# Kernel tuning notes

Measured on AMD Instinct MI355X. Metric: run time of the kernel, lower is better.

The kernel has to match this reference:

```python
import jax, jax.numpy as jnp
import numpy as np

MARGIN = 1.0
N, D = 8192, 128
NUM_CLASSES = 43


def setup_inputs() -> dict:
    key = jax.random.key(0)
    kx, ky = jax.random.split(key)
    x = jax.random.normal(kx, (N, D), dtype=jnp.float32)
    y = jax.random.randint(ky, (N,), 0, NUM_CLASSES, dtype=jnp.int64)
    return {"x": x, "y": y}


def reference(x, y):
    # Pairwise squared distances between rows of x: [N, N].
    # Equivalent to the original tile/permute construction, but via GEMM:
    # ||a-b||^2 = ||a||^2 + ||b||^2 - 2 a.b
    sq = jnp.sum(x * x, axis=1)                      # [N]
    norms = sq[:, None] + sq[None, :] - 2.0 * (x @ x.T)  # [N, N]
    maxims = jnp.maximum(MARGIN - norms, 0.0)        # [N, N]

    # Same-label mask (1 where labels equal, 0 otherwise).
    equalities = (y[:, None] == y[None, :]).astype(norms.dtype)  # [N, N]
    eye = jnp.eye(x.shape[0], dtype=norms.dtype)

    pos_mask = equalities - eye       # positive pairs, excluding self
    neg_mask = 1.0 - equalities       # negative pairs

    pos_term = jnp.sum(pos_mask * norms) / jnp.sum(pos_mask)
    neg_term = jnp.sum(neg_mask * maxims) / jnp.sum(neg_mask)
    return (pos_term + neg_term) / 2.0
```

## Files before the change

kernel.cpp:

```cpp
#include <hip/hip_runtime.h>

#define N_ROWS 8192
#define DIM 128
#define NCLS 43
#define TILE 256
#define TILES2 32
#define NPAIRS2 528

typedef __attribute__((ext_vector_type(8))) __bf16 bf16x8;
typedef __attribute__((ext_vector_type(4))) float float4v;
typedef __attribute__((address_space(1))) const void global_cvoid;
typedef __attribute__((address_space(3))) void lds_void;

__device__ __forceinline__ unsigned short f2bf(float f) {
    unsigned int u = __float_as_uint(f);
    u += 0x7FFFu + ((u >> 16) & 1u);
    return (unsigned short)(u >> 16);
}

__global__ void __launch_bounds__(256) prep_kernel(
        const float* __restrict__ x,
        float* __restrict__ sq,
        unsigned short* __restrict__ xbf) {
    int wave = threadIdx.x >> 6;
    int lane = threadIdx.x & 63;
    int row  = blockIdx.x * 4 + wave;
    const float2 v = *(const float2*)(x + (size_t)row * DIM + lane * 2);
    ushort2 b; b.x = f2bf(v.x); b.y = f2bf(v.y);
    *(ushort2*)(xbf + (size_t)row * DIM + lane * 2) = b;
    float s = v.x * v.x + v.y * v.y;
    #pragma unroll
    for (int off = 32; off > 0; off >>= 1) s += __shfl_down(s, off);
    if (lane == 0) sq[row] = s;
}

#define SM_B   65536
#define SM_SQA 131072
#define SM_SQB 132096
#define SM_YA  133120
#define SM_YB  134144
#define SM_RED 135168

__global__ void __launch_bounds__(1024, 4) tile_kernel(
        const unsigned short* __restrict__ xbf,
        const float* __restrict__ sq,
        const int* __restrict__ y,
        float2* __restrict__ partials) {
    __shared__ __align__(16) char smem[135296];

    int t = blockIdx.x;
    int bi = (int)((65.0f - sqrtf((float)(65 * 65 - 8 * t))) * 0.5f);
    if (bi < 0) bi = 0;
    if (bi > TILES2 - 1) bi = TILES2 - 1;
    while (bi * TILES2 - (bi * (bi - 1)) / 2 > t) --bi;
    while ((bi + 1) * TILES2 - ((bi + 1) * bi) / 2 <= t) ++bi;
    int bj = bi + (t - (bi * TILES2 - (bi * (bi - 1)) / 2));

    int wv   = threadIdx.x >> 6;
    int lane = threadIdx.x & 63;

    const char* srcA = (const char*)(xbf + (size_t)bi * TILE * DIM);
    const char* srcB = (const char*)(xbf + (size_t)bj * TILE * DIM);
    #pragma unroll
    for (int it = 0; it < 4; ++it) {
        int pbase = (it * 16 + wv) * 1024;
        int p = pbase + lane * 16;
        int r = p >> 8;
        int c = ((p >> 4) & 15) ^ (r & 15);
        int goff = (r << 8) + (c << 4);
        __builtin_amdgcn_global_load_lds(
            (global_cvoid*)(srcA + goff), (lds_void*)(smem + pbase), 16, 0, 0);
        __builtin_amdgcn_global_load_lds(
            (global_cvoid*)(srcB + goff), (lds_void*)(smem + SM_B + pbase), 16, 0, 0);
    }
    {
        int ti = threadIdx.x;
        if (ti < 256)       ((float*)(smem + SM_SQA))[ti]       = sq[bi * TILE + ti];
        else if (ti < 512)  ((float*)(smem + SM_SQB))[ti - 256] = sq[bj * TILE + ti - 256];
        else if (ti < 768)  ((int*)  (smem + SM_YA ))[ti - 512] = y [bi * TILE + ti - 512];
        else                ((int*)  (smem + SM_YB ))[ti - 768] = y [bj * TILE + ti - 768];
    }
    __syncthreads();

    int m    = lane & 15;
    int quad = lane >> 4;
    int wr   = (wv >> 2) * 64;
    int wc   = (wv & 3) * 64;

    float4v acc[4][4];
    #pragma unroll
    for (int a = 0; a < 4; ++a)
        #pragma unroll
        for (int b = 0; b < 4; ++b) {
            float4v z = {0.f, 0.f, 0.f, 0.f};
            acc[a][b] = z;
        }

    #pragma unroll
    for (int ks = 0; ks < 4; ++ks) {
        int chunk = ((ks * 4 + quad) ^ m) * 16;
        bf16x8 af[4], bfr[4];
        #pragma unroll
        for (int ti = 0; ti < 4; ++ti)
            af[ti] = *(const bf16x8*)(smem + (wr + ti * 16 + m) * 256 + chunk);
        #pragma unroll
        for (int tj = 0; tj < 4; ++tj)
            bfr[tj] = *(const bf16x8*)(smem + SM_B + (wc + tj * 16 + m) * 256 + chunk);
        #pragma unroll
        for (int ti = 0; ti < 4; ++ti)
            #pragma unroll
            for (int tj = 0; tj < 4; ++tj)
                acc[ti][tj] = __builtin_amdgcn_mfma_f32_16x16x32_bf16(
                                  af[ti], bfr[tj], acc[ti][tj], 0, 0, 0);
    }

    const float* sqA = (const float*)(smem + SM_SQA);
    const float* sqB = (const float*)(smem + SM_SQB);
    const int*   yA  = (const int*)  (smem + SM_YA);
    const int*   yB  = (const int*)  (smem + SM_YB);
    int ibase = wr + quad * 4;
    int jbase = wc + m;

    float sqj[4]; int yj[4];
    #pragma unroll
    for (int tj = 0; tj < 4; ++tj) {
        sqj[tj] = sqB[jbase + tj * 16];
        yj[tj]  = yB [jbase + tj * 16];
    }
    float posP = 0.f, negP = 0.f;
    if (bi != bj) {
        #pragma unroll
        for (int ti = 0; ti < 4; ++ti) {
            #pragma unroll
            for (int r = 0; r < 4; ++r) {
                int il = ibase + ti * 16 + r;
                float sqi = sqA[il];
                int   yi  = yA [il];
                #pragma unroll
                for (int tj = 0; tj < 4; ++tj) {
                    float nrm = fmaf(-2.0f, acc[ti][tj][r], sqi + sqj[tj]);
                    posP += (yi == yj[tj]) ? nrm : 0.f;
                    negP += fmaxf(1.0f - nrm, 0.f);
                }
            }
        }
        posP *= 2.0f; negP *= 2.0f;
    } else {
        #pragma unroll
        for (int ti = 0; ti < 4; ++ti) {
            #pragma unroll
            for (int r = 0; r < 4; ++r) {
                int il = ibase + ti * 16 + r;
                float sqi = sqA[il];
                int   yi  = yA [il];
                #pragma unroll
                for (int tj = 0; tj < 4; ++tj) {
                    int jl = jbase + tj * 16;
                    float nrm = fmaf(-2.0f, acc[ti][tj][r], sqi + sqj[tj]);
                    bool self = (il == jl);
                    posP += (yi == yj[tj] && !self) ? nrm : 0.f;
                    negP += self ? 0.f : fmaxf(1.0f - nrm, 0.f);
                }
            }
        }
    }

    #pragma unroll
    for (int off = 32; off > 0; off >>= 1) {
        posP += __shfl_down(posP, off);
        negP += __shfl_down(negP, off);
    }
    float2* wred = (float2*)(smem + SM_RED);
    if (lane == 0) wred[wv] = make_float2(posP, negP);
    __syncthreads();
    if (threadIdx.x == 0) {
        float ps = 0.f, ns = 0.f;
        #pragma unroll
        for (int w = 0; w < 16; ++w) { ps += wred[w].x; ns += wred[w].y; }
        partials[t] = make_float2(ps, ns);
    }
}

__global__ void __launch_bounds__(1024) finish_kernel(
        const float2* __restrict__ partials,
        const int* __restrict__ y,
        float* __restrict__ out) {
    __shared__ int hists[16][48];
    __shared__ float2 red[16];
    int tid = threadIdx.x, wv = tid >> 6, lane = tid & 63;

    for (int i = tid; i < 16 * 48; i += 1024) ((int*)hists)[i] = 0;
    __syncthreads();

    const int4* y4 = (const int4*)y;
    #pragma unroll
    for (int it = 0; it < 2; ++it) {
        int4 v = y4[tid + it * 1024];
        atomicAdd(&hists[wv][v.x], 1); atomicAdd(&hists[wv][v.y], 1);
        atomicAdd(&hists[wv][v.z], 1); atomicAdd(&hists[wv][v.w], 1);
    }

    float p = 0.f, n = 0.f;
    if (tid < NPAIRS2) { float2 v = partials[tid]; p = v.x; n = v.y; }
    #pragma unroll
    for (int off = 32; off > 0; off >>= 1) {
        p += __shfl_down(p, off);
        n += __shfl_down(n, off);
    }
    if (lane == 0) red[wv] = make_float2(p, n);
    __syncthreads();

    if (wv == 0) {
        int nc = 0;
        if (lane < NCLS) {
            #pragma unroll
            for (int w = 0; w < 16; ++w) nc += hists[w][lane];
        }
        int s2 = nc * nc;
        float pp = (lane < 16) ? red[lane].x : 0.f;
        float nn = (lane < 16) ? red[lane].y : 0.f;
        #pragma unroll
        for (int off = 32; off > 0; off >>= 1) {
            s2 += __shfl_down(s2, off);
            pp += __shfl_down(pp, off);
            nn += __shfl_down(nn, off);
        }
        if (lane == 0) {
            float posc = (float)(s2 - N_ROWS);
            float negc = (float)((long long)N_ROWS * N_ROWS - (long long)s2);
            out[0] = 0.5f * (pp / posc + nn / negc);
        }
    }
}

extern "C" void kernel_launch(void* const* d_in, const int* in_sizes, int n_in,
                              void* d_out, int out_size, void* d_ws, size_t ws_size,
                              hipStream_t stream) {
    const float* x = (const float*)d_in[0];
    const int*   y = (const int*)d_in[1];
    float* out = (float*)d_out;

    char* ws = (char*)d_ws;
    float2*         partials = (float2*)ws;
    float*          sq       = (float*)(ws + 4352);
    unsigned short* xbf      = (unsigned short*)(ws + 37120);

    prep_kernel<<<N_ROWS / 4, 256, 0, stream>>>(x, sq, xbf);
    tile_kernel<<<NPAIRS2, 1024, 0, stream>>>(xbf, sq, y, partials);
    finish_kernel<<<1, 1024, 0, stream>>>(partials, y, out);
}
```

Measured before the change: 83.28 us.

## Persistent tile loop with bound-based hinge skip and fused final reduction

```diff
diff --git a/kernel.cpp b/kernel.cpp
--- a/kernel.cpp
+++ b/kernel.cpp
@@ -6,59 +6,37 @@
 #define TILE 256
 #define TILES2 32
 #define NPAIRS2 528
+#define NBLOCKS 256
 
 typedef __attribute__((ext_vector_type(8))) __bf16 bf16x8;
 typedef __attribute__((ext_vector_type(4))) float float4v;
 typedef __attribute__((address_space(1))) const void global_cvoid;
 typedef __attribute__((address_space(3))) void lds_void;
 
+#define SM_B    65536
+#define SM_SQY  131072
+#define SM_RED  139264
+#define SM_FLAG 139456
+#define SM_SIZE 139520
+
 __device__ __forceinline__ unsigned short f2bf(float f) {
     unsigned int u = __float_as_uint(f);
     u += 0x7FFFu + ((u >> 16) & 1u);
     return (unsigned short)(u >> 16);
 }
 
-__global__ void __launch_bounds__(256) prep_kernel(
-        const float* __restrict__ x,
-        float* __restrict__ sq,
-        unsigned short* __restrict__ xbf) {
-    int wave = threadIdx.x >> 6;
-    int lane = threadIdx.x & 63;
-    int row  = blockIdx.x * 4 + wave;
-    const float2 v = *(const float2*)(x + (size_t)row * DIM + lane * 2);
-    ushort2 b; b.x = f2bf(v.x); b.y = f2bf(v.y);
-    *(ushort2*)(xbf + (size_t)row * DIM + lane * 2) = b;
-    float s = v.x * v.x + v.y * v.y;
-    #pragma unroll
-    for (int off = 32; off > 0; off >>= 1) s += __shfl_down(s, off);
-    if (lane == 0) sq[row] = s;
-}
-
-#define SM_B   65536
-#define SM_SQA 131072
-#define SM_SQB 132096
-#define SM_YA  133120
-#define SM_YB  134144
-#define SM_RED 135168
-
-__global__ void __launch_bounds__(1024, 4) tile_kernel(
-        const unsigned short* __restrict__ xbf,
-        const float* __restrict__ sq,
-        const int* __restrict__ y,
-        float2* __restrict__ partials) {
-    __shared__ __align__(16) char smem[135296];
-
-    int t = blockIdx.x;
-    int bi = (int)((65.0f - sqrtf((float)(65 * 65 - 8 * t))) * 0.5f);
-    if (bi < 0) bi = 0;
-    if (bi > TILES2 - 1) bi = TILES2 - 1;
-    while (bi * TILES2 - (bi * (bi - 1)) / 2 > t) --bi;
-    while ((bi + 1) * TILES2 - ((bi + 1) * bi) / 2 <= t) ++bi;
-    int bj = bi + (t - (bi * TILES2 - (bi * (bi - 1)) / 2));
-
-    int wv   = threadIdx.x >> 6;
-    int lane = threadIdx.x & 63;
-
+__device__ __forceinline__ void decode_tile(int t, int& bi, int& bj) {
+    int b = (int)((65.0f - sqrtf((float)(65 * 65 - 8 * t))) * 0.5f);
+    if (b < 0) b = 0;
+    if (b > TILES2 - 1) b = TILES2 - 1;
+    while (b * TILES2 - (b * (b - 1)) / 2 > t) --b;
+    while ((b + 1) * TILES2 - ((b + 1) * b) / 2 <= t) ++b;
+    bi = b; bj = b + (t - (b * TILES2 - (b * (b - 1)) / 2));
+}
+
+__device__ __forceinline__ void stage_tile(
+        const unsigned short* xbf, const float* sq, const int* y,
+        char* smem, int bi, int bj, int par, int wv, int lane) {
     const char* srcA = (const char*)(xbf + (size_t)bi * TILE * DIM);
     const char* srcB = (const char*)(xbf + (size_t)bj * TILE * DIM);
     #pragma unroll
@@ -73,163 +51,245 @@
         __builtin_amdgcn_global_load_lds(
             (global_cvoid*)(srcB + goff), (lds_void*)(smem + SM_B + pbase), 16, 0, 0);
     }
-    {
-        int ti = threadIdx.x;
-        if (ti < 256)       ((float*)(smem + SM_SQA))[ti]       = sq[bi * TILE + ti];
-        else if (ti < 512)  ((float*)(smem + SM_SQB))[ti - 256] = sq[bj * TILE + ti - 256];
-        else if (ti < 768)  ((int*)  (smem + SM_YA ))[ti - 512] = y [bi * TILE + ti - 512];
-        else                ((int*)  (smem + SM_YB ))[ti - 768] = y [bj * TILE + ti - 768];
-    }
-    __syncthreads();
-
+    if (wv < 4) {
+        const char* src = (wv == 0) ? (const char*)(sq + bi * TILE)
+                        : (wv == 1) ? (const char*)(sq + bj * TILE)
+                        : (wv == 2) ? (const char*)(y  + bi * TILE)
+                                    : (const char*)(y  + bj * TILE);
+        __builtin_amdgcn_global_load_lds(
+            (global_cvoid*)(src + lane * 16),
+            (lds_void*)(smem + SM_SQY + par * 4096 + wv * 1024), 16, 0, 0);
+    }
+}
+
+__global__ void __launch_bounds__(256) prep_kernel(
+        const float* __restrict__ x,
+        float* __restrict__ sq,
+        unsigned short* __restrict__ xbf,
+        int* __restrict__ counter) {
+    if (blockIdx.x == 0 && threadIdx.x == 0) *counter = 0;
+    int wave = threadIdx.x >> 6;
+    int lane = threadIdx.x & 63;
+    int half = lane >> 5, l32 = lane & 31;
+    int row  = blockIdx.x * 8 + wave * 2 + half;
+    const float4 v = *(const float4*)(x + (size_t)row * DIM + l32 * 4);
+    ushort4 b; b.x = f2bf(v.x); b.y = f2bf(v.y); b.z = f2bf(v.z); b.w = f2bf(v.w);
+    *(ushort4*)(xbf + (size_t)row * DIM + l32 * 4) = b;
+    float s = v.x * v.x + v.y * v.y + v.z * v.z + v.w * v.w;
+    #pragma unroll
+    for (int off = 16; off > 0; off >>= 1) s += __shfl_down(s, off);
+    if (l32 == 0) sq[row] = s;
+}
+
+__global__ void __launch_bounds__(1024, 4) tile_kernel(
+        const unsigned short* __restrict__ xbf,
+        const float* __restrict__ sq,
+        const int* __restrict__ y,
+        float2* __restrict__ partials,
+        int* __restrict__ counter,
+        float* __restrict__ out) {
+    __shared__ __align__(16) char smem[SM_SIZE];
+
+    int b    = blockIdx.x;
+    int wv   = threadIdx.x >> 6;
+    int lane = threadIdx.x & 63;
     int m    = lane & 15;
     int quad = lane >> 4;
     int wr   = (wv >> 2) * 64;
     int wc   = (wv & 3) * 64;
-
-    float4v acc[4][4];
-    #pragma unroll
-    for (int a = 0; a < 4; ++a)
-        #pragma unroll
-        for (int b = 0; b < 4; ++b) {
-            float4v z = {0.f, 0.f, 0.f, 0.f};
-            acc[a][b] = z;
-        }
-
-    #pragma unroll
-    for (int ks = 0; ks < 4; ++ks) {
-        int chunk = ((ks * 4 + quad) ^ m) * 16;
-        bf16x8 af[4], bfr[4];
-        #pragma unroll
-        for (int ti = 0; ti < 4; ++ti)
-            af[ti] = *(const bf16x8*)(smem + (wr + ti * 16 + m) * 256 + chunk);
-        #pragma unroll
-        for (int tj = 0; tj < 4; ++tj)
-            bfr[tj] = *(const bf16x8*)(smem + SM_B + (wc + tj * 16 + m) * 256 + chunk);
-        #pragma unroll
-        for (int ti = 0; ti < 4; ++ti)
-            #pragma unroll
-            for (int tj = 0; tj < 4; ++tj)
-                acc[ti][tj] = __builtin_amdgcn_mfma_f32_16x16x32_bf16(
-                                  af[ti], bfr[tj], acc[ti][tj], 0, 0, 0);
-    }
-
-    const float* sqA = (const float*)(smem + SM_SQA);
-    const float* sqB = (const float*)(smem + SM_SQB);
-    const int*   yA  = (const int*)  (smem + SM_YA);
-    const int*   yB  = (const int*)  (smem + SM_YB);
     int ibase = wr + quad * 4;
     int jbase = wc + m;
 
-    float sqj[4]; int yj[4];
-    #pragma unroll
-    for (int tj = 0; tj < 4; ++tj) {
-        sqj[tj] = sqB[jbase + tj * 16];
-        yj[tj]  = yB [jbase + tj * 16];
-    }
-    float posP = 0.f, negP = 0.f;
-    if (bi != bj) {
-        #pragma unroll
-        for (int ti = 0; ti < 4; ++ti) {
-            #pragma unroll
-            for (int r = 0; r < 4; ++r) {
-                int il = ibase + ti * 16 + r;
-                float sqi = sqA[il];
-                int   yi  = yA [il];
+    float posAcc = 0.f, negAcc = 0.f;
+    int parity = 0;
+
+    {
+        int bi, bj; decode_tile(b, bi, bj);
+        stage_tile(xbf, sq, y, smem, bi, bj, 0, wv, lane);
+    }
+    __syncthreads();
+
+    for (int t = b; t < NPAIRS2; t += NBLOCKS) {
+        int bi, bj; decode_tile(t, bi, bj);
+
+        float4v acc[4][4];
+        #pragma unroll
+        for (int a = 0; a < 4; ++a)
+            #pragma unroll
+            for (int c = 0; c < 4; ++c) {
+                float4v z = {0.f, 0.f, 0.f, 0.f};
+                acc[a][c] = z;
+            }
+
+        #pragma unroll
+        for (int ks = 0; ks < 4; ++ks) {
+            int chunk = ((ks * 4 + quad) ^ m) * 16;
+            bf16x8 af[4], bfr[4];
+            #pragma unroll
+            for (int ti = 0; ti < 4; ++ti)
+                af[ti] = *(const bf16x8*)(smem + (wr + ti * 16 + m) * 256 + chunk);
+            #pragma unroll
+            for (int tj = 0; tj < 4; ++tj)
+                bfr[tj] = *(const bf16x8*)(smem + SM_B + (wc + tj * 16 + m) * 256 + chunk);
+            #pragma unroll
+            for (int ti = 0; ti < 4; ++ti)
                 #pragma unroll
-                for (int tj = 0; tj < 4; ++tj) {
-                    float nrm = fmaf(-2.0f, acc[ti][tj][r], sqi + sqj[tj]);
-                    posP += (yi == yj[tj]) ? nrm : 0.f;
-                    negP += fmaxf(1.0f - nrm, 0.f);
+                for (int tj = 0; tj < 4; ++tj)
+                    acc[ti][tj] = __builtin_amdgcn_mfma_f32_16x16x32_bf16(
+                                      af[ti], bfr[tj], acc[ti][tj], 0, 0, 0);
+        }
+        __syncthreads();
+
+        int tn = t + NBLOCKS;
+        if (tn < NPAIRS2) {
+            int nbi, nbj; decode_tile(tn, nbi, nbj);
+            stage_tile(xbf, sq, y, smem, nbi, nbj, parity ^ 1, wv, lane);
+        }
+
+        const float* sqA = (const float*)(smem + SM_SQY + parity * 4096);
+        const float* sqB = sqA + 256;
+        const int*   yA  = (const int*)(sqA + 512);
+        const int*   yB  = (const int*)(sqA + 768);
+
+        float sqj[4]; int yj[4];
+        #pragma unroll
+        for (int tj = 0; tj < 4; ++tj) {
+            sqj[tj] = sqB[jbase + tj * 16];
+            yj[tj]  = yB [jbase + tj * 16];
+        }
+        float sqjmin = fminf(fminf(sqj[0], sqj[1]), fminf(sqj[2], sqj[3]));
+        float posD = 0.f, dotmax = -3e38f, sqimin = 3e38f;
+
+        if (bi != bj) {
+            #pragma unroll
+            for (int ti = 0; ti < 4; ++ti) {
+                #pragma unroll
+                for (int r = 0; r < 4; ++r) {
+                    int il = ibase + ti * 16 + r;
+                    float sqi = sqA[il]; int yi = yA[il];
+                    sqimin = fminf(sqimin, sqi);
+                    #pragma unroll
+                    for (int tj = 0; tj < 4; ++tj) {
+                        float d = acc[ti][tj][r];
+                        posD += (yi == yj[tj]) ? d : 0.f;
+                        dotmax = fmaxf(dotmax, d);
+                    }
                 }
             }
-        }
-        posP *= 2.0f; negP *= 2.0f;
-    } else {
-        #pragma unroll
-        for (int ti = 0; ti < 4; ++ti) {
-            #pragma unroll
-            for (int r = 0; r < 4; ++r) {
-                int il = ibase + ti * 16 + r;
-                float sqi = sqA[il];
-                int   yi  = yA [il];
+        } else {
+            #pragma unroll
+            for (int ti = 0; ti < 4; ++ti) {
                 #pragma unroll
-                for (int tj = 0; tj < 4; ++tj) {
-                    int jl = jbase + tj * 16;
-                    float nrm = fmaf(-2.0f, acc[ti][tj][r], sqi + sqj[tj]);
-                    bool self = (il == jl);
-                    posP += (yi == yj[tj] && !self) ? nrm : 0.f;
-                    negP += self ? 0.f : fmaxf(1.0f - nrm, 0.f);
+                for (int r = 0; r < 4; ++r) {
+                    int il = ibase + ti * 16 + r;
+                    float sqi = sqA[il]; int yi = yA[il];
+                    sqimin = fminf(sqimin, sqi);
+                    #pragma unroll
+                    for (int tj = 0; tj < 4; ++tj) {
+                        int jl = jbase + tj * 16;
+                        bool self = (il == jl);
+                        float d = acc[ti][tj][r];
+                        posD += (yi == yj[tj] && !self) ? d : 0.f;
+                        dotmax = fmaxf(dotmax, self ? -3e38f : d);
+                    }
                 }
             }
         }
+
+        float negS = 0.f;
+        if (2.f * dotmax - sqimin - sqjmin >= -1.f) {
+            #pragma unroll
+            for (int ti = 0; ti < 4; ++ti)
+                #pragma unroll
+                for (int r = 0; r < 4; ++r) {
+                    int il = ibase + ti * 16 + r;
+                    float sqi = sqA[il]; int yi = yA[il];
+                    #pragma unroll
+                    for (int tj = 0; tj < 4; ++tj)
+                        if (yi != yj[tj]) {
+                            float nrm = fmaf(-2.f, acc[ti][tj][r], sqi + sqj[tj]);
+                            negS += fmaxf(1.f - nrm, 0.f);
+                        }
+                }
+        }
+        float wgt = (bi == bj) ? 1.f : 2.f;
+        posAcc += wgt * posD;
+        negAcc += wgt * negS;
+
+        parity ^= 1;
+        __syncthreads();
     }
 
     #pragma unroll
     for (int off = 32; off > 0; off >>= 1) {
-        posP += __shfl_down(posP, off);
-        negP += __shfl_down(negP, off);
-    }
-    float2* wred = (float2*)(smem + SM_RED);
-    if (lane == 0) wred[wv] = make_float2(posP, negP);
+        posAcc += __shfl_down(posAcc, off);
+        negAcc += __shfl_down(negAcc, off);
+    }
+    float2* pred  = (float2*)(smem + SM_RED);
+    float*  swred = (float*)(smem + SM_RED + 128);
+    int*    flag  = (int*)(smem + SM_FLAG);
+    if (lane == 0) pred[wv] = make_float2(posAcc, negAcc);
     __syncthreads();
     if (threadIdx.x == 0) {
         float ps = 0.f, ns = 0.f;
         #pragma unroll
-        for (int w = 0; w < 16; ++w) { ps += wred[w].x; ns += wred[w].y; }
-        partials[t] = make_float2(ps, ns);
-    }
-}
-
-__global__ void __launch_bounds__(1024) finish_kernel(
-        const float2* __restrict__ partials,
-        const int* __restrict__ y,
-        float* __restrict__ out) {
-    __shared__ int hists[16][48];
-    __shared__ float2 red[16];
-    int tid = threadIdx.x, wv = tid >> 6, lane = tid & 63;
-
-    for (int i = tid; i < 16 * 48; i += 1024) ((int*)hists)[i] = 0;
+        for (int w = 0; w < 16; ++w) { ps += pred[w].x; ns += pred[w].y; }
+        partials[b] = make_float2(ps, ns);
+        __threadfence();
+        int old = atomicAdd(counter, 1);
+        *flag = (old == NBLOCKS - 1) ? 1 : 0;
+    }
+    __syncthreads();
+    if (*flag == 0) return;
+
+    __threadfence();
+    int tid = threadIdx.x;
+    int* hists = (int*)smem;
+    int* htot  = (int*)smem + 16 * 48;
+    for (int i = tid; i < 16 * 48 + 48; i += 1024) ((int*)smem)[i] = 0;
     __syncthreads();
 
     const int4* y4 = (const int4*)y;
-    #pragma unroll
-    for (int it = 0; it < 2; ++it) {
-        int4 v = y4[tid + it * 1024];
-        atomicAdd(&hists[wv][v.x], 1); atomicAdd(&hists[wv][v.y], 1);
-        atomicAdd(&hists[wv][v.z], 1); atomicAdd(&hists[wv][v.w], 1);
-    }
+    int4 ya = y4[tid], yb = y4[tid + 1024];
+    atomicAdd(&hists[wv * 48 + ya.x], 1); atomicAdd(&hists[wv * 48 + ya.y], 1);
+    atomicAdd(&hists[wv * 48 + ya.z], 1); atomicAdd(&hists[wv * 48 + ya.w], 1);
+    atomicAdd(&hists[wv * 48 + yb.x], 1); atomicAdd(&hists[wv * 48 + yb.y], 1);
+    atomicAdd(&hists[wv * 48 + yb.z], 1); atomicAdd(&hists[wv * 48 + yb.w], 1);
+    __syncthreads();
+    if (tid < 48) {
+        int nc = 0;
+        #pragma unroll
+        for (int w = 0; w < 16; ++w) nc += hists[w * 48 + tid];
+        htot[tid] = nc;
+    }
+    __syncthreads();
+
+    const float4* sq4 = (const float4*)sq;
+    float4 sa = sq4[tid], sb = sq4[tid + 1024];
+    float sw = sa.x * (float)(htot[ya.x] - 1) + sa.y * (float)(htot[ya.y] - 1)
+             + sa.z * (float)(htot[ya.z] - 1) + sa.w * (float)(htot[ya.w] - 1)
+             + sb.x * (float)(htot[yb.x] - 1) + sb.y * (float)(htot[yb.y] - 1)
+             + sb.z * (float)(htot[yb.z] - 1) + sb.w * (float)(htot[yb.w] - 1);
 
     float p = 0.f, n = 0.f;
-    if (tid < NPAIRS2) { float2 v = partials[tid]; p = v.x; n = v.y; }
+    if (tid < NBLOCKS) { float2 v = partials[tid]; p = v.x; n = v.y; }
     #pragma unroll
     for (int off = 32; off > 0; off >>= 1) {
-        p += __shfl_down(p, off);
-        n += __shfl_down(n, off);
-    }
-    if (lane == 0) red[wv] = make_float2(p, n);
-    __syncthreads();
-
-    if (wv == 0) {
-        int nc = 0;
-        if (lane < NCLS) {
-            #pragma unroll
-            for (int w = 0; w < 16; ++w) nc += hists[w][lane];
-        }
-        int s2 = nc * nc;
-        float pp = (lane < 16) ? red[lane].x : 0.f;
-        float nn = (lane < 16) ? red[lane].y : 0.f;
-        #pragma unroll
-        for (int off = 32; off > 0; off >>= 1) {
-            s2 += __shfl_down(s2, off);
-            pp += __shfl_down(pp, off);
-            nn += __shfl_down(nn, off);
-        }
-        if (lane == 0) {
-            float posc = (float)(s2 - N_ROWS);
-            float negc = (float)((long long)N_ROWS * N_ROWS - (long long)s2);
-            out[0] = 0.5f * (pp / posc + nn / negc);
-        }
+        sw += __shfl_down(sw, off);
+        p  += __shfl_down(p, off);
+        n  += __shfl_down(n, off);
+    }
+    if (lane == 0) { pred[wv] = make_float2(p, n); swred[wv] = sw; }
+    __syncthreads();
+    if (tid == 0) {
+        float PS = 0.f, NS = 0.f, SW = 0.f;
+        #pragma unroll
+        for (int w = 0; w < 16; ++w) { PS += pred[w].x; NS += pred[w].y; SW += swred[w]; }
+        long long s2 = 0;
+        for (int c = 0; c < NCLS; ++c) { long long h = htot[c]; s2 += h * h; }
+        float posc = (float)(s2 - (long long)N_ROWS);
+        float negc = (float)((long long)N_ROWS * N_ROWS - s2);
+        out[0] = 0.5f * ((2.f * SW - 2.f * PS) / posc + NS / negc);
     }
 }
 
@@ -242,10 +302,10 @@
 
     char* ws = (char*)d_ws;
     float2*         partials = (float2*)ws;
-    float*          sq       = (float*)(ws + 4352);
-    unsigned short* xbf      = (unsigned short*)(ws + 37120);
-
-    prep_kernel<<<N_ROWS / 4, 256, 0, stream>>>(x, sq, xbf);
-    tile_kernel<<<NPAIRS2, 1024, 0, stream>>>(xbf, sq, y, partials);
-    finish_kernel<<<1, 1024, 0, stream>>>(partials, y, out);
-}
+    int*            counter  = (int*)(ws + 2048);
+    float*          sq       = (float*)(ws + 2560);
+    unsigned short* xbf      = (unsigned short*)(ws + 35328);
+
+    prep_kernel<<<N_ROWS / 8, 256, 0, stream>>>(x, sq, xbf, counter);
+    tile_kernel<<<NBLOCKS, 1024, 0, stream>>>(xbf, sq, y, partials, counter, out);
+}
```

Result: slower. 88.41 us (+6.2%).
